# Kernel tuning notes

Measured on AMD Instinct MI355X. Metric: run time of the kernel, lower is better.

The kernel has to match this reference:

```python
import jax, jax.numpy as jnp
import numpy as np

N_NODES = 20000
N_EDGES = 320000
IN_C = 256
HID = 32
HEADS0 = 4  # n_heads[0]: both #modules in first layer and heads per module
OUT_C = 40
NEG_SLOPE = 0.2


def _segment_softmax(e, seg, n):
    # e: [E, H], softmax over edges grouped by destination node
    m = jax.ops.segment_max(e, seg, num_segments=n)
    m = jnp.where(jnp.isfinite(m), m, 0.0)  # nodes with no in-edges
    ex = jnp.exp(e - m[seg])
    s = jax.ops.segment_sum(ex, seg, num_segments=n)
    return ex / (s[seg] + 1e-16)


def _gat_conv(x, W, a_src, a_dst, bias, src, dst, n, concat):
    # PyG GATConv math (self-loops assumed already appended to src/dst)
    H, C = a_src.shape
    h = (x @ W).reshape(n, H, C)                      # [N, H, C]
    e_src = (h * a_src).sum(-1)                       # [N, H]
    e_dst = (h * a_dst).sum(-1)                       # [N, H]
    e = jax.nn.leaky_relu(e_src[src] + e_dst[dst], NEG_SLOPE)  # [E, H]
    alpha = _segment_softmax(e, dst, n)               # [E, H]
    out = jax.ops.segment_sum(h[src] * alpha[:, :, None], dst, num_segments=n)
    if concat:
        return out.reshape(n, H * C) + bias
    return out.mean(axis=1) + bias


def setup_inputs() -> dict:
    key = jax.random.key(0)
    ks = jax.random.split(key, 12)
    x = jax.random.normal(ks[0], (N_NODES, IN_C), dtype=jnp.float32)
    edge_index = jax.random.randint(ks[1], (2, N_EDGES), 0, N_NODES, dtype=jnp.int32)
    M = HEADS0  # number of first-layer modules
    W1 = jax.random.normal(ks[2], (M, IN_C, HEADS0 * HID), dtype=jnp.float32) * 0.1
    a_src1 = jax.random.normal(ks[3], (M, HEADS0, HID), dtype=jnp.float32) * 0.1
    a_dst1 = jax.random.normal(ks[4], (M, HEADS0, HID), dtype=jnp.float32) * 0.1
    b1 = jax.random.normal(ks[5], (M, HEADS0 * HID), dtype=jnp.float32) * 0.1
    cat_dim = M * HEADS0 * HID  # 512: actual width after torch.cat over modules
    W2 = jax.random.normal(ks[6], (cat_dim, OUT_C), dtype=jnp.float32) * 0.1
    a_src2 = jax.random.normal(ks[7], (1, OUT_C), dtype=jnp.float32) * 0.1
    a_dst2 = jax.random.normal(ks[8], (1, OUT_C), dtype=jnp.float32) * 0.1
    b2 = jax.random.normal(ks[9], (OUT_C,), dtype=jnp.float32) * 0.1
    return {"x": x, "edge_index": edge_index, "W1": W1, "a_src1": a_src1,
            "a_dst1": a_dst1, "b1": b1, "W2": W2, "a_src2": a_src2,
            "a_dst2": a_dst2, "b2": b2}


def reference(x, edge_index, W1, a_src1, a_dst1, b1, W2, a_src2, a_dst2, b2):
    n = x.shape[0]
    loops = jnp.arange(n, dtype=edge_index.dtype)  # PyG add_self_loops=True
    src = jnp.concatenate([edge_index[0], loops])
    dst = jnp.concatenate([edge_index[1], loops])
    # first layer: HEADS0 independent GATConv modules, outputs concatenated
    outs = jax.vmap(lambda W, a_s, a_d, b: _gat_conv(x, W, a_s, a_d, b, src, dst, n, True))(
        W1, a_src1, a_dst1, b1)                      # [M, N, HEADS0*HID]
    h = jnp.transpose(outs, (1, 0, 2)).reshape(n, -1)  # [N, 512]
    h = jax.nn.elu(h)  # dropout is a no-op in eval mode
    out = _gat_conv(h, W2, a_src2, a_dst2, b2, src, dst, n, False)  # [N, OUT_C]
    return jax.nn.log_softmax(out, axis=1)
```

## Files before the change

### kernel.cpp

```cpp
#include <hip/hip_runtime.h>
#include <cstdint>
#include <cstddef>

#define N_NODES 20000
#define N_EDGES 320000
#define E_TOT   340000
#define IN_C    256
#define HID     32
#define HEADS0  4
#define OUT_C   40
#define NEG_SLOPE 0.2f
#define CAT     512
#define MH      16
#define H2S     48

typedef unsigned short ushort_t;
typedef __attribute__((ext_vector_type(8))) short short8v;
typedef __attribute__((ext_vector_type(4))) float f32x4;
typedef __attribute__((ext_vector_type(8))) unsigned short ushort8v;

#define WAVE_FENCE() asm volatile("" ::: "memory")

__device__ inline float bf2f(unsigned short u) {
  union { unsigned int i; float f; } c; c.i = ((unsigned int)u) << 16; return c.f;
}
__device__ inline unsigned short f2bf(float f) {
  union { float f; unsigned int i; } c; c.f = f;
  unsigned int r = c.i + 0x7FFFu + ((c.i >> 16) & 1u);
  return (unsigned short)(r >> 16);
}

#define XCB  (N_NODES * IN_C / 8 / 256)
#define DEGB ((E_TOT + 255) / 256)

__global__ __launch_bounds__(256) void prep_k(const float* __restrict__ x,
                                              ushort_t* __restrict__ xb,
                                              const float* __restrict__ W1,
                                              ushort_t* __restrict__ bhi,
                                              ushort_t* __restrict__ blo,
                                              const float* __restrict__ W2,
                                              ushort_t* __restrict__ b2hi,
                                              ushort_t* __restrict__ b2lo,
                                              const int* __restrict__ ei,
                                              int* __restrict__ deg) {
  int blk = blockIdx.x;
  if (blk < XCB) {
    int i = blk * 256 + threadIdx.x;
    const float4* xp = (const float4*)(x + (size_t)i * 8);
    float4 f0 = xp[0], f1 = xp[1];
    float v[8] = {f0.x, f0.y, f0.z, f0.w, f1.x, f1.y, f1.z, f1.w};
    ushort8v o;
#pragma unroll
    for (int j = 0; j < 8; j++) o[j] = f2bf(v[j]);
    *(ushort8v*)(xb + (size_t)i * 8) = o;
  } else if (blk < XCB + 64) {
    int idx = (blk - XCB) * 256 + threadIdx.x;
    int n16  = idx >> 9;
    int k32  = (idx >> 6) & 7;
    int lane = idx & 63;
    int cfull = n16 * 16 + (lane & 15);
    int m = cfull >> 7;
    int c = cfull & 127;
    int kbase = k32 * 32 + (lane >> 4) * 8;
#pragma unroll
    for (int b = 0; b < 8; b++) {
      float v = W1[((m << 8) + kbase + b) * 128 + c];
      ushort_t h = f2bf(v);
      bhi[(size_t)idx * 8 + b] = h;
      blo[(size_t)idx * 8 + b] = f2bf(v - bf2f(h));
    }
  } else if (blk < XCB + 76) {
    int idx = (blk - XCB - 64) * 256 + threadIdx.x;
    int n16  = idx >> 10;
    int k32  = (idx >> 6) & 15;
    int lane = idx & 63;
    int n = n16 * 16 + (lane & 15);
    int kbase = k32 * 32 + (lane >> 4) * 8;
#pragma unroll
    for (int b = 0; b < 8; b++) {
      float v = (n < OUT_C) ? W2[(kbase + b) * OUT_C + n] : 0.f;
      ushort_t h = f2bf(v);
      b2hi[(size_t)idx * 8 + b] = h;
      b2lo[(size_t)idx * 8 + b] = f2bf(v - bf2f(h));
    }
  } else {
    int e = (blk - XCB - 76) * 256 + threadIdx.x;
    if (e < E_TOT) {
      int d = (e < N_EDGES) ? ei[N_EDGES + e] : (e - N_EDGES);
      atomicAdd(&deg[d], 1);
    }
  }
}

__global__ __launch_bounds__(1024) void scan_k(const int* __restrict__ deg, int* __restrict__ row_ptr) {
  const int C = 20;
  __shared__ int part[1024];
  int t = threadIdx.x;
  int b = t * C;
  int s = 0;
  for (int i = 0; i < C; i++) { int idx = b + i; if (idx < N_NODES) s += deg[idx]; }
  part[t] = s;
  __syncthreads();
  for (int off = 1; off < 1024; off <<= 1) {
    int v = part[t];
    int u = (t >= off) ? part[t - off] : 0;
    __syncthreads();
    part[t] = v + u;
    __syncthreads();
  }
  int run = (t > 0) ? part[t - 1] : 0;
  for (int i = 0; i < C; i++) {
    int idx = b + i;
    if (idx <= N_NODES) {
      row_ptr[idx] = run;
      if (idx < N_NODES) run += deg[idx];
    }
  }
}

__global__ __launch_bounds__(256) void scatter_score_k(const int* __restrict__ ei,
                                                       const int* __restrict__ row_ptr,
                                                       int* __restrict__ fill,
                                                       int* __restrict__ csr_src,
                                                       const float* __restrict__ es1,
                                                       const float* __restrict__ ed1,
                                                       ushort_t* __restrict__ exq) {
  int e = blockIdx.x * 256 + threadIdx.x;
  if (e >= E_TOT) return;
  int s, d;
  if (e < N_EDGES) { s = ei[e]; d = ei[N_EDGES + e]; }
  else             { s = e - N_EDGES; d = s; }
  int pos = row_ptr[d] + atomicAdd(&fill[d], 1);
  csr_src[pos] = s;

  const float4* sp = (const float4*)(es1 + (size_t)s * MH);
  const float4* dp = (const float4*)(ed1 + (size_t)d * MH);
  float4 a0 = sp[0], a1 = sp[1], a2 = sp[2], a3 = sp[3];
  float4 b0 = dp[0], b1 = dp[1], b2 = dp[2], b3 = dp[3];
  float v[16] = {a0.x + b0.x, a0.y + b0.y, a0.z + b0.z, a0.w + b0.w,
                 a1.x + b1.x, a1.y + b1.y, a1.z + b1.z, a1.w + b1.w,
                 a2.x + b2.x, a2.y + b2.y, a2.z + b2.z, a2.w + b2.w,
                 a3.x + b3.x, a3.y + b3.y, a3.z + b3.z, a3.w + b3.w};
  ushort8v o0, o1;
#pragma unroll
  for (int i = 0; i < 16; i++) {
    float ev = v[i];
    ev = (ev > 0.f) ? ev : ev * NEG_SLOPE;
    float ex = __expf(ev);
    if (i < 8) o0[i] = f2bf(ex); else o1[i - 8] = f2bf(ex);
  }
  *(ushort8v*)(exq + (size_t)pos * MH)     = o0;
  *(ushort8v*)(exq + (size_t)pos * MH + 8) = o1;
}

__global__ __launch_bounds__(256) void gemm1_mfma_k(const ushort_t* __restrict__ xb,
                                                    const ushort_t* __restrict__ bhi,
                                                    const ushort_t* __restrict__ blo,
                                                    const float* __restrict__ a_src1,
                                                    const float* __restrict__ a_dst1,
                                                    ushort_t* __restrict__ h1b,
                                                    float* __restrict__ es1,
                                                    float* __restrict__ ed1) {
  int tid = threadIdx.x;
  int wave = tid >> 6, lane = tid & 63;
  int l15 = lane & 15, lhi = lane >> 4;
  int wrow = blockIdx.x * 64 + (wave & 1) * 32;
  int wcol = blockIdx.y * 128 + (wave >> 1) * 64;
  int n16base = wcol >> 4;

  f32x4 acc[2][4];
#pragma unroll
  for (int mf = 0; mf < 2; mf++)
#pragma unroll
    for (int nf = 0; nf < 4; nf++) acc[mf][nf] = (f32x4){0.f, 0.f, 0.f, 0.f};

  int arow[2];
#pragma unroll
  for (int mf = 0; mf < 2; mf++) {
    int r = wrow + mf * 16 + l15;
    arow[mf] = (r < N_NODES) ? r : (N_NODES - 1);
  }

  for (int ks = 0; ks < 8; ks++) {
    short8v ah[2];
#pragma unroll
    for (int mf = 0; mf < 2; mf++)
      ah[mf] = *(const short8v*)(xb + (size_t)arow[mf] * IN_C + ks * 32 + lhi * 8);
    short8v bh[4], bl[4];
#pragma unroll
    for (int nf = 0; nf < 4; nf++) {
      size_t boff = ((size_t)((n16base + nf) * 8 + ks) * 64 + lane) * 8;
      bh[nf] = *(const short8v*)(bhi + boff);
      bl[nf] = *(const short8v*)(blo + boff);
    }
#pragma unroll
    for (int mf = 0; mf < 2; mf++)
#pragma unroll
      for (int nf = 0; nf < 4; nf++) {
        acc[mf][nf] = __builtin_amdgcn_mfma_f32_16x16x32_bf16(ah[mf], bh[nf], acc[mf][nf], 0, 0, 0);
        acc[mf][nf] = __builtin_amdgcn_mfma_f32_16x16x32_bf16(ah[mf], bl[nf], acc[mf][nf], 0, 0, 0);
      }
  }

#pragma unroll
  for (int mf = 0; mf < 2; mf++) {
    int rbase = wrow + mf * 16 + lhi * 4;
#pragma unroll
    for (int nf = 0; nf < 4; nf++) {
      int col = wcol + nf * 16 + l15;
#pragma unroll
      for (int r = 0; r < 4; r++) {
        int row = rbase + r;
        if (row < N_NODES)
          h1b[(size_t)row * CAT + col] = f2bf(acc[mf][nf][r]);
      }
    }
  }

  int mh0 = wcol >> 5;
  float as[4], ad[4];
#pragma unroll
  for (int nf = 0; nf < 4; nf++) {
    int aidx = (mh0 + (nf >> 1)) * HID + (nf & 1) * 16 + l15;
    as[nf] = a_src1[aidx];
    ad[nf] = a_dst1[aidx];
  }
#pragma unroll
  for (int mf = 0; mf < 2; mf++) {
#pragma unroll
    for (int r = 0; r < 4; r++) {
      int row = wrow + mf * 16 + lhi * 4 + r;
      float ps0 = acc[mf][0][r] * as[0] + acc[mf][1][r] * as[1];
      float ps1 = acc[mf][2][r] * as[2] + acc[mf][3][r] * as[3];
      float pd0 = acc[mf][0][r] * ad[0] + acc[mf][1][r] * ad[1];
      float pd1 = acc[mf][2][r] * ad[2] + acc[mf][3][r] * ad[3];
#pragma unroll
      for (int msk = 1; msk < 16; msk <<= 1) {
        ps0 += __shfl_xor(ps0, msk); ps1 += __shfl_xor(ps1, msk);
        pd0 += __shfl_xor(pd0, msk); pd1 += __shfl_xor(pd1, msk);
      }
      if (l15 == 0 && row < N_NODES) {
        es1[row * MH + mh0]     = ps0;
        es1[row * MH + mh0 + 1] = ps1;
        ed1[row * MH + mh0]     = pd0;
        ed1[row * MH + mh0 + 1] = pd1;
      }
    }
  }
}


__global__ __launch_bounds__(256) void agg1_k(const ushort_t* __restrict__ h1b,
                                              const ushort_t* __restrict__ exq,
                                              const int* __restrict__ row_ptr,
                                              const int* __restrict__ csr_src,
                                              const float* __restrict__ b1,
                                              ushort_t* __restrict__ h1e) {
  int w = threadIdx.x >> 6, lane = threadIdx.x & 63;
  int n = blockIdx.x * 4 + w;
  int beg = row_ptr[n];
  int deg = row_ptr[n + 1] - beg;
  int hh = lane >> 2;

  __shared__ float ex_buf[4][64][MH + 1];
  __shared__ int   src_buf[4][64];

  float s_part[MH];
#pragma unroll
  for (int i = 0; i < MH; i++) s_part[i] = 0.f;
  float acc[8];
#pragma unroll
  for (int j = 0; j < 8; j++) acc[j] = 0.f;

  for (int base = 0; base < deg; base += 64) {
    int cnt = min(64, deg - base);
    if (lane < cnt) {
      int p = beg + base + lane;
      src_buf[w][lane] = csr_src[p];
      ushort8v q0 = *(const ushort8v*)(exq + (size_t)p * MH);
      ushort8v q1 = *(const ushort8v*)(exq + (size_t)p * MH + 8);
#pragma unroll
      for (int i = 0; i < 8; i++) {
        float ex = bf2f(q0[i]);
        ex_buf[w][lane][i] = ex;
        s_part[i] += ex;
      }
#pragma unroll
      for (int i = 0; i < 8; i++) {
        float ex = bf2f(q1[i]);
        ex_buf[w][lane][8 + i] = ex;
        s_part[8 + i] += ex;
      }
    }
    WAVE_FENCE();
    int e = 0;
    for (; e + 3 < cnt; e += 4) {
      int s0 = src_buf[w][e + 0], s1 = src_buf[w][e + 1];
      int s2 = src_buf[w][e + 2], s3 = src_buf[w][e + 3];
      float x0 = ex_buf[w][e + 0][hh], x1 = ex_buf[w][e + 1][hh];
      float x2 = ex_buf[w][e + 2][hh], x3 = ex_buf[w][e + 3][hh];
      ushort8v v0 = *(const ushort8v*)(h1b + (size_t)s0 * CAT + lane * 8);
      ushort8v v1 = *(const ushort8v*)(h1b + (size_t)s1 * CAT + lane * 8);
      ushort8v v2 = *(const ushort8v*)(h1b + (size_t)s2 * CAT + lane * 8);
      ushort8v v3 = *(const ushort8v*)(h1b + (size_t)s3 * CAT + lane * 8);
#pragma unroll
      for (int j = 0; j < 8; j++) acc[j] += x0 * bf2f(v0[j]);
#pragma unroll
      for (int j = 0; j < 8; j++) acc[j] += x1 * bf2f(v1[j]);
#pragma unroll
      for (int j = 0; j < 8; j++) acc[j] += x2 * bf2f(v2[j]);
#pragma unroll
      for (int j = 0; j < 8; j++) acc[j] += x3 * bf2f(v3[j]);
    }
    for (; e < cnt; e++) {
      int s = src_buf[w][e];
      float xv = ex_buf[w][e][hh];
      ushort8v hv = *(const ushort8v*)(h1b + (size_t)s * CAT + lane * 8);
#pragma unroll
      for (int j = 0; j < 8; j++) acc[j] += xv * bf2f(hv[j]);
    }
    WAVE_FENCE();
  }

  float denom = 0.f;
#pragma unroll
  for (int i = 0; i < MH; i++) {
    float v = s_part[i];
    v += __shfl_xor(v, 1);  v += __shfl_xor(v, 2);  v += __shfl_xor(v, 4);
    v += __shfl_xor(v, 8);  v += __shfl_xor(v, 16); v += __shfl_xor(v, 32);
    if (hh == i) denom = v;
  }
  denom += 1e-16f;

  const float4* b1p = (const float4*)(b1 + lane * 8);
  float4 bq0 = b1p[0], bq1 = b1p[1];
  float bv8[8] = {bq0.x, bq0.y, bq0.z, bq0.w, bq1.x, bq1.y, bq1.z, bq1.w};

  ushort8v vhi;
#pragma unroll
  for (int j = 0; j < 8; j++) {
    float o = acc[j] / denom + bv8[j];
    float e = (o > 0.f) ? o : (__expf(o) - 1.f);
    vhi[j] = f2bf(e);
  }
  *(ushort8v*)(h1e + (size_t)n * CAT + lane * 8) = vhi;
}

__global__ __launch_bounds__(256) void gemm2_mfma_k(const ushort_t* __restrict__ h1e,
                                                    const ushort_t* __restrict__ b2hi,
                                                    const ushort_t* __restrict__ b2lo,
                                                    const float* __restrict__ a_src2,
                                                    const float* __restrict__ a_dst2,
                                                    ushort_t* __restrict__ h2b,
                                                    float* __restrict__ es2,
                                                    float* __restrict__ ed2) {
  int tid = threadIdx.x;
  int wave = tid >> 6, lane = tid & 63;
  int l15 = lane & 15, lhi = lane >> 4;
  int wrow = blockIdx.x * 64 + wave * 16;

  f32x4 acc[3];
#pragma unroll
  for (int nf = 0; nf < 3; nf++) acc[nf] = (f32x4){0.f, 0.f, 0.f, 0.f};

  int r0 = wrow + l15;
  int arow = (r0 < N_NODES) ? r0 : (N_NODES - 1);

  for (int ks = 0; ks < 16; ks++) {
    size_t aoff = (size_t)arow * CAT + ks * 32 + lhi * 8;
    short8v ah = *(const short8v*)(h1e + aoff);
#pragma unroll
    for (int nf = 0; nf < 3; nf++) {
      size_t boff = ((size_t)(nf * 16 + ks) * 64 + lane) * 8;
      short8v bh = *(const short8v*)(b2hi + boff);
      short8v bl = *(const short8v*)(b2lo + boff);
      acc[nf] = __builtin_amdgcn_mfma_f32_16x16x32_bf16(ah, bh, acc[nf], 0, 0, 0);
      acc[nf] = __builtin_amdgcn_mfma_f32_16x16x32_bf16(ah, bl, acc[nf], 0, 0, 0);
    }
  }

  float av[3], bv[3];
#pragma unroll
  for (int nf = 0; nf < 3; nf++) {
    int col = nf * 16 + l15;
    av[nf] = (col < OUT_C) ? a_src2[col] : 0.f;
    bv[nf] = (col < OUT_C) ? a_dst2[col] : 0.f;
  }
#pragma unroll
  for (int r = 0; r < 4; r++) {
    int row = wrow + lhi * 4 + r;
    float ps = acc[0][r] * av[0] + acc[1][r] * av[1] + acc[2][r] * av[2];
    float pd = acc[0][r] * bv[0] + acc[1][r] * bv[1] + acc[2][r] * bv[2];
    ps += __shfl_xor(ps, 1); pd += __shfl_xor(pd, 1);
    ps += __shfl_xor(ps, 2); pd += __shfl_xor(pd, 2);
    ps += __shfl_xor(ps, 4); pd += __shfl_xor(pd, 4);
    ps += __shfl_xor(ps, 8); pd += __shfl_xor(pd, 8);
    if (row < N_NODES) {
#pragma unroll
      for (int nf = 0; nf < 3; nf++)
        h2b[(size_t)row * H2S + nf * 16 + l15] = f2bf(acc[nf][r]);
      if (l15 == 0) { es2[row] = ps; ed2[row] = pd; }
    }
  }
}

__global__ __launch_bounds__(256) void agg2_k(const ushort_t* __restrict__ h2b,
                                              const float* __restrict__ es2,
                                              const float* __restrict__ ed2,
                                              const int* __restrict__ row_ptr,
                                              const int* __restrict__ csr_src,
                                              const float* __restrict__ b2,
                                              float* __restrict__ out) {
  int w = threadIdx.x >> 6, lane = threadIdx.x & 63;
  int n = blockIdx.x * 4 + w;
  int beg = row_ptr[n];
  int deg = row_ptr[n + 1] - beg;
  float edn = ed2[n];

  __shared__ float exb[4][64];
  __shared__ int   srb[4][64];

  float acc = 0.f, ssum = 0.f;
  for (int base = 0; base < deg; base += 64) {
    int cnt = min(64, deg - base);
    if (lane < cnt) {
      int s = csr_src[beg + base + lane];
      srb[w][lane] = s;
      float ev = es2[s] + edn;
      ev = (ev > 0.f) ? ev : ev * NEG_SLOPE;
      float ex = __expf(ev);
      exb[w][lane] = ex;
      ssum += ex;
    }
    WAVE_FENCE();
    int e = 0;
    for (; e + 3 < cnt; e += 4) {
      int s0 = srb[w][e], s1 = srb[w][e + 1], s2 = srb[w][e + 2], s3 = srb[w][e + 3];
      float x0 = exb[w][e], x1 = exb[w][e + 1], x2 = exb[w][e + 2], x3 = exb[w][e + 3];
      if (lane < OUT_C) {
        float v0 = bf2f(h2b[(size_t)s0 * H2S + lane]);
        float v1 = bf2f(h2b[(size_t)s1 * H2S + lane]);
        float v2 = bf2f(h2b[(size_t)s2 * H2S + lane]);
        float v3 = bf2f(h2b[(size_t)s3 * H2S + lane]);
        acc += x0 * v0; acc += x1 * v1; acc += x2 * v2; acc += x3 * v3;
      }
    }
    for (; e < cnt; e++) {
      int s = srb[w][e];
      float xv = exb[w][e];
      if (lane < OUT_C) acc += xv * bf2f(h2b[(size_t)s * H2S + lane]);
    }
    WAVE_FENCE();
  }

  ssum += __shfl_xor(ssum, 1); ssum += __shfl_xor(ssum, 2); ssum += __shfl_xor(ssum, 4);
  ssum += __shfl_xor(ssum, 8); ssum += __shfl_xor(ssum, 16); ssum += __shfl_xor(ssum, 32);

  float val = (lane < OUT_C) ? (acc / (ssum + 1e-16f) + b2[lane]) : -INFINITY;

  float rmax = val;
#pragma unroll
  for (int o = 1; o < 64; o <<= 1) rmax = fmaxf(rmax, __shfl_xor(rmax, o));
  float ex = (lane < OUT_C) ? __expf(val - rmax) : 0.f;
  float sume = ex;
#pragma unroll
  for (int o = 1; o < 64; o <<= 1) sume += __shfl_xor(sume, o);
  if (lane < OUT_C) out[(size_t)n * OUT_C + lane] = val - rmax - __logf(sume);
}


extern "C" void kernel_launch(void* const* d_in, const int* in_sizes, int n_in,
                              void* d_out, int out_size, void* d_ws, size_t ws_size,
                              hipStream_t stream) {
  const float* x      = (const float*)d_in[0];
  const int*   ei     = (const int*)d_in[1];
  const float* W1     = (const float*)d_in[2];
  const float* a_src1 = (const float*)d_in[3];
  const float* a_dst1 = (const float*)d_in[4];
  const float* b1     = (const float*)d_in[5];
  const float* W2     = (const float*)d_in[6];
  const float* a_src2 = (const float*)d_in[7];
  const float* a_dst2 = (const float*)d_in[8];
  const float* b2     = (const float*)d_in[9];
  float* out = (float*)d_out;

  char* ws = (char*)d_ws;
  size_t off = 0;
  auto alloc = [&](size_t bytes) -> void* {
    void* p = ws + off;
    off += (bytes + 255) & ~(size_t)255;
    return p;
  };
  ushort_t* xb   = (ushort_t*)alloc((size_t)N_NODES * IN_C * 2);
  ushort_t* bhi  = (ushort_t*)alloc((size_t)32 * 8 * 64 * 8 * 2);
  ushort_t* blo  = (ushort_t*)alloc((size_t)32 * 8 * 64 * 8 * 2);
  ushort_t* b2hi = (ushort_t*)alloc((size_t)3 * 16 * 64 * 8 * 2);
  ushort_t* b2lo = (ushort_t*)alloc((size_t)3 * 16 * 64 * 8 * 2);
  ushort_t* h1b  = (ushort_t*)alloc((size_t)N_NODES * CAT * 2);
  ushort_t* h1e  = (ushort_t*)alloc((size_t)N_NODES * CAT * 2);
  ushort_t* exq  = (ushort_t*)alloc((size_t)E_TOT * MH * 2);
  float* es1     = (float*)alloc((size_t)N_NODES * MH * 4);
  float* ed1     = (float*)alloc((size_t)N_NODES * MH * 4);
  ushort_t* h2b  = (ushort_t*)alloc((size_t)N_NODES * H2S * 2);
  float* es2     = (float*)alloc((size_t)N_NODES * 4);
  float* ed2     = (float*)alloc((size_t)N_NODES * 4);
  int*   deg     = (int*)alloc((size_t)N_NODES * 4);
  int*   fill    = (int*)alloc((size_t)N_NODES * 4);
  int*   row_ptr = (int*)alloc((size_t)(N_NODES + 1) * 4);
  int*   csr_src = (int*)alloc((size_t)E_TOT * 4);

  hipMemsetAsync(deg, 0, (((size_t)N_NODES * 4 + 255) & ~(size_t)255) + (size_t)N_NODES * 4, stream);

  prep_k<<<XCB + 76 + DEGB, 256, 0, stream>>>(x, xb, W1, bhi, blo, W2, b2hi, b2lo, ei, deg);
  scan_k<<<1, 1024, 0, stream>>>(deg, row_ptr);
  gemm1_mfma_k<<<dim3((N_NODES + 63) / 64, CAT / 128), 256, 0, stream>>>(
      xb, bhi, blo, a_src1, a_dst1, h1b, es1, ed1);
  scatter_score_k<<<(E_TOT + 255) / 256, 256, 0, stream>>>(
      ei, row_ptr, fill, csr_src, es1, ed1, exq);
  agg1_k<<<N_NODES / 4, 256, 0, stream>>>(h1b, exq, row_ptr, csr_src, b1, h1e);
  gemm2_mfma_k<<<(N_NODES + 63) / 64, 256, 0, stream>>>(h1e, b2hi, b2lo, a_src2, a_dst2, h2b, es2, ed2);
  agg2_k<<<N_NODES / 4, 256, 0, stream>>>(h2b, es2, ed2, row_ptr, csr_src, b2, out);
}
```

Before: 184.9 us.

## Swizzle gemm1 block order and split-K gemm2 across waves with LDS reduction

gemm1 now runs on a 1D grid and remaps block ids so that 8 consecutive row tiles share their 4 column blocks, which should improve L2 reuse of A and B tiles; blocks past the last row tile exit early. gemm2 changes from 64 rows per block with the full K loop per wave to 16 rows per block, with each of the four waves handling a quarter of K. Partial sums are reduced through shared memory and finished by wave 0. The aim is more blocks for the small N=40 GEMM and so better occupancy and latency hiding, at the cost of a barrier, LDS traffic and one idle-ish reducing wave.

New measurement: 182.8 us. Within noise of the previous version (-1.2%).

```diff
diff --git a/kernel.cpp b/kernel.cpp
--- a/kernel.cpp
+++ b/kernel.cpp
@@ -161,11 +161,16 @@
                                                     ushort_t* __restrict__ h1b,
                                                     float* __restrict__ es1,
                                                     float* __restrict__ ed1) {
+  int id = blockIdx.x;
+  int row8 = ((id >> 5) << 3) | (id & 7);
+  int colb = (id >> 3) & 3;
+  if (row8 > 312) return;
+
   int tid = threadIdx.x;
   int wave = tid >> 6, lane = tid & 63;
   int l15 = lane & 15, lhi = lane >> 4;
-  int wrow = blockIdx.x * 64 + (wave & 1) * 32;
-  int wcol = blockIdx.y * 128 + (wave >> 1) * 64;
+  int wrow = row8 * 64 + (wave & 1) * 32;
+  int wcol = colb * 128 + (wave >> 1) * 64;
   int n16base = wcol >> 4;
 
   f32x4 acc[2][4];
@@ -357,16 +362,19 @@
   int tid = threadIdx.x;
   int wave = tid >> 6, lane = tid & 63;
   int l15 = lane & 15, lhi = lane >> 4;
-  int wrow = blockIdx.x * 64 + wave * 16;
+  int wrow = blockIdx.x * 16;
+
+  __shared__ f32x4 part[4][3][64];
 
   f32x4 acc[3];
 #pragma unroll
   for (int nf = 0; nf < 3; nf++) acc[nf] = (f32x4){0.f, 0.f, 0.f, 0.f};
 
-  int r0 = wrow + l15;
-  int arow = (r0 < N_NODES) ? r0 : (N_NODES - 1);
-
-  for (int ks = 0; ks < 16; ks++) {
+  int arow = wrow + l15;
+
+#pragma unroll
+  for (int kk = 0; kk < 4; kk++) {
+    int ks = wave * 4 + kk;
     size_t aoff = (size_t)arow * CAT + ks * 32 + lhi * 8;
     short8v ah = *(const short8v*)(h1e + aoff);
 #pragma unroll
@@ -379,26 +387,38 @@
     }
   }
 
-  float av[3], bv[3];
-#pragma unroll
-  for (int nf = 0; nf < 3; nf++) {
-    int col = nf * 16 + l15;
-    av[nf] = (col < OUT_C) ? a_src2[col] : 0.f;
-    bv[nf] = (col < OUT_C) ? a_dst2[col] : 0.f;
-  }
-#pragma unroll
-  for (int r = 0; r < 4; r++) {
-    int row = wrow + lhi * 4 + r;
-    float ps = acc[0][r] * av[0] + acc[1][r] * av[1] + acc[2][r] * av[2];
-    float pd = acc[0][r] * bv[0] + acc[1][r] * bv[1] + acc[2][r] * bv[2];
-    ps += __shfl_xor(ps, 1); pd += __shfl_xor(pd, 1);
-    ps += __shfl_xor(ps, 2); pd += __shfl_xor(pd, 2);
-    ps += __shfl_xor(ps, 4); pd += __shfl_xor(pd, 4);
-    ps += __shfl_xor(ps, 8); pd += __shfl_xor(pd, 8);
-    if (row < N_NODES) {
+#pragma unroll
+  for (int nf = 0; nf < 3; nf++) part[wave][nf][lane] = acc[nf];
+  __syncthreads();
+
+  if (wave == 0) {
+    f32x4 tot[3];
+#pragma unroll
+    for (int nf = 0; nf < 3; nf++) {
+      f32x4 p0 = part[0][nf][lane], p1 = part[1][nf][lane];
+      f32x4 p2 = part[2][nf][lane], p3 = part[3][nf][lane];
+      tot[nf] = (p0 + p1) + (p2 + p3);
+    }
+
+    float av[3], bv[3];
+#pragma unroll
+    for (int nf = 0; nf < 3; nf++) {
+      int col = nf * 16 + l15;
+      av[nf] = (col < OUT_C) ? a_src2[col] : 0.f;
+      bv[nf] = (col < OUT_C) ? a_dst2[col] : 0.f;
+    }
+#pragma unroll
+    for (int r = 0; r < 4; r++) {
+      int row = wrow + lhi * 4 + r;
+      float ps = tot[0][r] * av[0] + tot[1][r] * av[1] + tot[2][r] * av[2];
+      float pd = tot[0][r] * bv[0] + tot[1][r] * bv[1] + tot[2][r] * bv[2];
+      ps += __shfl_xor(ps, 1); pd += __shfl_xor(pd, 1);
+      ps += __shfl_xor(ps, 2); pd += __shfl_xor(pd, 2);
+      ps += __shfl_xor(ps, 4); pd += __shfl_xor(pd, 4);
+      ps += __shfl_xor(ps, 8); pd += __shfl_xor(pd, 8);
 #pragma unroll
       for (int nf = 0; nf < 3; nf++)
-        h2b[(size_t)row * H2S + nf * 16 + l15] = f2bf(acc[nf][r]);
+        h2b[(size_t)row * H2S + nf * 16 + l15] = f2bf(tot[nf][r]);
       if (l15 == 0) { es2[row] = ps; ed2[row] = pd; }
     }
   }
@@ -513,11 +533,11 @@
 
   prep_k<<<XCB + 76 + DEGB, 256, 0, stream>>>(x, xb, W1, bhi, blo, W2, b2hi, b2lo, ei, deg);
   scan_k<<<1, 1024, 0, stream>>>(deg, row_ptr);
-  gemm1_mfma_k<<<dim3((N_NODES + 63) / 64, CAT / 128), 256, 0, stream>>>(
+  gemm1_mfma_k<<<1280, 256, 0, stream>>>(
       xb, bhi, blo, a_src1, a_dst1, h1b, es1, ed1);
   scatter_score_k<<<(E_TOT + 255) / 256, 256, 0, stream>>>(
       ei, row_ptr, fill, csr_src, es1, ed1, exq);
   agg1_k<<<N_NODES / 4, 256, 0, stream>>>(h1b, exq, row_ptr, csr_src, b1, h1e);
-  gemm2_mfma_k<<<(N_NODES + 63) / 64, 256, 0, stream>>>(h1e, b2hi, b2lo, a_src2, a_dst2, h2b, es2, ed2);
+  gemm2_mfma_k<<<N_NODES / 16, 256, 0, stream>>>(h1e, b2hi, b2lo, a_src2, a_dst2, h2b, es2, ed2);
   agg2_k<<<N_NODES / 4, 256, 0, stream>>>(h2b, es2, ed2, row_ptr, csr_src, b2, out);
 }
```
